# Performance work log

Hardware: AMD Instinct MI355X
Metric: run time of the kernel (lower is better)

Reference implementation:

```python
import jax, jax.numpy as jnp
import numpy as np

B, T, C, L = 1024, 1024, 96, 32
BLANK = C - 1          # tf.compat.v1.nn.ctc_loss uses num_classes-1 as blank
S = 2 * L + 1          # extended label length (blanks interleaved)
NEG = -1e30            # log-space 'zero'


def setup_inputs() -> dict:
    key = jax.random.key(0)
    k1, k2 = jax.random.split(key)
    y_true = jax.random.randint(k1, (B, L), 0, BLANK).astype(jnp.int64)  # labels in [0, C-2]
    y_pred = jax.random.normal(k2, (B, T, C), dtype=jnp.float32)          # pre-softmax logits
    return {"y_true": y_true, "y_pred": y_pred}


def _ctc_loss(y_pred, y_true):
    # y_pred: [B,T,C] logits, y_true: [B,L] int labels. All lengths are full
    # (label_length = L, input_length = T), matching the layer's call().
    logp = jax.nn.log_softmax(y_pred, axis=-1)                   # [B,T,C]
    # extended labels: blank, l0, blank, l1, ..., blank  -> [B,S]
    ext = jnp.full((B, S), BLANK, dtype=jnp.int32).at[:, 1::2].set(y_true.astype(jnp.int32))
    # skip transition allowed where ext[s] != blank and ext[s] != ext[s-2]
    skip = jnp.concatenate(
        [jnp.zeros((B, 2), bool), (ext[:, 2:] != BLANK) & (ext[:, 2:] != ext[:, :-2])],
        axis=1)                                                  # [B,S]
    # per-time emission log-probs of extended labels: [T,B,S]
    lp_ext = jnp.take_along_axis(logp, ext[:, None, :], axis=2)  # [B,T,S]
    lp_ext = jnp.transpose(lp_ext, (1, 0, 2))                    # [T,B,S]

    alpha0 = (jnp.full((B, S), NEG, dtype=logp.dtype)
              .at[:, 0].set(lp_ext[0, :, 0])
              .at[:, 1].set(lp_ext[0, :, 1]))

    def step(alpha, lp_t):
        a_stay = alpha
        a_prev = jnp.concatenate([jnp.full((B, 1), NEG, alpha.dtype), alpha[:, :-1]], axis=1)
        a_skip = jnp.concatenate([jnp.full((B, 2), NEG, alpha.dtype), alpha[:, :-2]], axis=1)
        a_skip = jnp.where(skip, a_skip, NEG)
        m = jnp.maximum(jnp.maximum(a_stay, a_prev), a_skip)
        new = m + jnp.log(jnp.exp(a_stay - m) + jnp.exp(a_prev - m) + jnp.exp(a_skip - m))
        return new + lp_t, None

    alphaT, _ = jax.lax.scan(step, alpha0, lp_ext[1:])
    # total log-likelihood ends at last blank or last label
    end = jnp.stack([alphaT[:, S - 1], alphaT[:, S - 2]], axis=0)  # [2,B]
    loss = -jax.scipy.special.logsumexp(end, axis=0)               # [B]
    return loss[:, None]                                           # [B,1], as ctc_batch_cost


def reference(y_true, y_pred):
    return _ctc_loss(y_pred, y_true)
```

## Files before the change

kernel.cpp:

```cpp
#include <hip/hip_runtime.h>


#define NB 1024
#define NT 1024
#define NC 96
#define NL 32
#define NEGF (-1e30f)
#define CHUNK 32
#define NCHUNK (NT / CHUNK)
#define SLOTF 97
#define LOG2E 1.4426950408889634f
#define LN2   0.69314718055994531f

__device__ __forceinline__ float fexp2(float x) { return __builtin_amdgcn_exp2f(x); }
__device__ __forceinline__ float flog2(float x) { return __builtin_amdgcn_logf(x); }

template <int CTRL>
__device__ __forceinline__ float dpp_mov(float v) {
  return __int_as_float(__builtin_amdgcn_update_dpp(
      __float_as_int(v), __float_as_int(v), CTRL, 0xF, 0xF, false));
}
__device__ __forceinline__ float dpp_shr1(float oldv, float v) {
  return __int_as_float(__builtin_amdgcn_update_dpp(
      __float_as_int(oldv), __float_as_int(v), 0x138, 0xF, 0xF, false));
}

__global__ __launch_bounds__(256) void ctc_fused(const int* __restrict__ yt,
                                                 const float* __restrict__ yp,
                                                 float* __restrict__ out) {
  __shared__ float ring[2 * CHUNK * SLOTF];

  const int b = blockIdx.x;
  const int wid = threadIdx.x >> 6;
  const int lane = threadIdx.x & 63;

  const float* __restrict__ xrow = yp + (size_t)b * NT * NC;

  const int cw = b & 3;
  const bool is_cons = (wid == cw);
  const int pr = ((wid - cw + 4) & 3) - 1;

  int extc = 95;
  bool skipf = false;
  if (is_cons) {
    const int* lab = yt + b * NL;
    if ((lane & 1) == 0) {
      const int j = lane >> 1;
      extc = lab[j];
      skipf = (j > 0) && (extc != lab[j - 1]);
    }
    __builtin_amdgcn_s_setprio(1);
  }

  const int rsel = lane >> 5;
  const int l32 = lane & 31;

  float UA[6][3], UB[6][3];

  auto load_regs = [&](float (&U)[6][3], int t0) {
    const float* rp = xrow + (size_t)(t0 + 2 * pr + rsel) * NC + l32;
#pragma unroll
    for (int jj = 0; jj < 6; ++jj) {
      if (pr + 3 * jj < 16) {
        U[jj][0] = rp[jj * 6 * NC + 0];
        U[jj][1] = rp[jj * 6 * NC + 32];
        U[jj][2] = rp[jj * 6 * NC + 64];
      }
    }
  };

  auto compute_store = [&](float (&U)[6][3], int cc) {
    float* wb = ring + (cc & 1) * (CHUNK * SLOTF) + (2 * pr + rsel) * SLOTF + l32;
#pragma unroll
    for (int jj = 0; jj < 6; ++jj) {
      if (pr + 3 * jj < 16) {
        const float u0 = U[jj][0] * LOG2E;
        const float u1 = U[jj][1] * LOG2E;
        const float u2 = U[jj][2] * LOG2E;
        float z = fexp2(u0) + fexp2(u1) + fexp2(u2);
        z += dpp_mov<0xB1>(z);
        z += dpp_mov<0x4E>(z);
        z += dpp_mov<0x124>(z);
        z += dpp_mov<0x128>(z);
        z += __shfl_xor(z, 16);
        const float lz = flog2(z);
        wb[jj * 6 * SLOTF + 0]  = u0 - lz;
        wb[jj * 6 * SLOTF + 32] = u1 - lz;
        wb[jj * 6 * SLOTF + 64] = u2 - lz;
      }
    }
  };

  float alpha = NEGF;
  float a0 = NEGF;

  auto consume = [&](int cc, bool first) {
    const float* hb = ring + (cc & 1) * (CHUNK * SLOTF) + extc;
    const float* hb95 = ring + (cc & 1) * (CHUNK * SLOTF) + 95;
    float lq[4], lqb[4];
    lq[0] = hb[0 * SLOTF];  lqb[0] = hb95[0 * SLOTF];
    lq[1] = hb[1 * SLOTF];  lqb[1] = hb95[1 * SLOTF];
    lq[2] = hb[2 * SLOTF];  lqb[2] = hb95[2 * SLOTF];
    lq[3] = 0.0f;           lqb[3] = 0.0f;
#pragma unroll
    for (int tt = 0; tt < CHUNK; ++tt) {
      const float lp = lq[tt & 3];
      const float lpb = lqb[tt & 3];
      if (tt + 3 < CHUNK) {
        lq[(tt + 3) & 3] = hb[(tt + 3) * SLOTF];
        lqb[(tt + 3) & 3] = hb95[(tt + 3) * SLOTF];
      }
      if (first && tt == 0) {
        a0 = lpb;
        alpha = (lane == 0) ? lp : NEGF;
      } else {
        const float ap = dpp_shr1(a0, alpha);
        float as = dpp_shr1(NEGF, ap);
        as = skipf ? as : NEGF;
        float mm, mid, mn;
        asm("v_max3_f32 %0, %1, %2, %3" : "=v"(mm) : "v"(alpha), "v"(ap), "v"(as));
        asm("v_med3_f32 %0, %1, %2, %3" : "=v"(mid) : "v"(alpha), "v"(ap), "v"(as));
        asm("v_min3_f32 %0, %1, %2, %3" : "=v"(mn) : "v"(alpha), "v"(ap), "v"(as));
        const float sm = (1.0f + fexp2(mid - mm)) + fexp2(mn - mm);
        alpha = (mm + lp) + flog2(sm);
        a0 += lpb;
      }
    }
  };

  if (!is_cons) load_regs(UA, 0);

  for (int c = 0; c < NCHUNK; c += 2) {
    if (!is_cons) {
      if (c + 1 < NCHUNK) load_regs(UB, (c + 1) * CHUNK);
      compute_store(UA, c);
      __syncthreads();
      if (c + 2 < NCHUNK) load_regs(UA, (c + 2) * CHUNK);
      compute_store(UB, c + 1);
      __syncthreads();
    } else {
      __syncthreads();
      if (c == 0) consume(0, true);
      else consume(c, false);
      __syncthreads();
      consume(c + 1, false);
    }
  }

  if (is_cons) {
    const float aS1 = __shfl(alpha, 63);
    const float aS2 = __shfl(alpha, 62);
    if (lane == 0) {
      const float mF = fmaxf(aS1, aS2);
      const float r = mF + flog2(fexp2(aS1 - mF) + fexp2(aS2 - mF));
      out[b] = -r * LN2;
    }
  }
}

extern "C" void kernel_launch(void* const* d_in, const int* in_sizes, int n_in,
                              void* d_out, int out_size, void* d_ws, size_t ws_size,
                              hipStream_t stream) {
  const int* yt = (const int*)d_in[0];
  const float* yp = (const float*)d_in[1];
  float* out = (float*)d_out;
  hipLaunchKernelGGL(ctc_fused, dim3(NB), dim3(256), 0, stream, yt, yp, out);
}
```

Measured before the change: 86.50 us.

## Gather extended-label log-probs in producers and store them as packed float2 rows

Measured after the change: 99.30 us. 14.8% more time.

```diff
diff --git a/kernel.cpp b/kernel.cpp
--- a/kernel.cpp
+++ b/kernel.cpp
@@ -8,7 +8,6 @@
 #define NEGF (-1e30f)
 #define CHUNK 32
 #define NCHUNK (NT / CHUNK)
-#define SLOTF 97
 #define LOG2E 1.4426950408889634f
 #define LN2   0.69314718055994531f
 
@@ -24,11 +23,17 @@
   return __int_as_float(__builtin_amdgcn_update_dpp(
       __float_as_int(oldv), __float_as_int(v), 0x138, 0xF, 0xF, false));
 }
+__device__ __forceinline__ float bperm(int byte_addr, float v) {
+  return __int_as_float(__builtin_amdgcn_ds_bpermute(byte_addr, __float_as_int(v)));
+}
+__device__ __forceinline__ float rdlane(float v, int l) {
+  return __int_as_float(__builtin_amdgcn_readlane(__float_as_int(v), l));
+}
 
 __global__ __launch_bounds__(256) void ctc_fused(const int* __restrict__ yt,
                                                  const float* __restrict__ yp,
                                                  float* __restrict__ out) {
-  __shared__ float ring[2 * CHUNK * SLOTF];
+  __shared__ float2 ring2[2 * CHUNK * 64];
 
   const int b = blockIdx.x;
   const int wid = threadIdx.x >> 6;
@@ -40,14 +45,19 @@
   const bool is_cons = (wid == cw);
   const int pr = ((wid - cw + 4) & 3) - 1;
 
-  int extc = 95;
+  const int* lab = yt + b * NL;
+  const int myl = lab[lane >> 1];
+  const int ea = ((lane & 1) == 0) ? myl : 95;
+  const bool e_hi = (ea >= 64);
+  const bool e_mid = (ea >= 32) && (ea < 64);
+  const int addrA = (ea & 31) << 2;
+  const int addrB = addrA + 128;
+
   bool skipf = false;
   if (is_cons) {
-    const int* lab = yt + b * NL;
     if ((lane & 1) == 0) {
       const int j = lane >> 1;
-      extc = lab[j];
-      skipf = (j > 0) && (extc != lab[j - 1]);
+      skipf = (j > 0) && (myl != lab[j - 1]);
     }
     __builtin_amdgcn_s_setprio(1);
   }
@@ -70,7 +80,7 @@
   };
 
   auto compute_store = [&](float (&U)[6][3], int cc) {
-    float* wb = ring + (cc & 1) * (CHUNK * SLOTF) + (2 * pr + rsel) * SLOTF + l32;
+    float2* wb = ring2 + (cc & 1) * (CHUNK * 64) + (2 * pr) * 64 + lane;
 #pragma unroll
     for (int jj = 0; jj < 6; ++jj) {
       if (pr + 3 * jj < 16) {
@@ -84,9 +94,27 @@
         z += dpp_mov<0x128>(z);
         z += __shfl_xor(z, 16);
         const float lz = flog2(z);
-        wb[jj * 6 * SLOTF + 0]  = u0 - lz;
-        wb[jj * 6 * SLOTF + 32] = u1 - lz;
-        wb[jj * 6 * SLOTF + 64] = u2 - lz;
+        const float v0 = u0 - lz, v1 = u1 - lz, v2 = u2 - lz;
+        {
+          const float r0 = bperm(addrA, v0), r1 = bperm(addrA, v1),
+                      r2 = bperm(addrA, v2);
+          float s = e_mid ? r1 : r0;
+          s = e_hi ? r2 : s;
+          float2 pr2;
+          pr2.x = s;
+          pr2.y = rdlane(v2, 31);
+          wb[jj * 6 * 64] = pr2;
+        }
+        {
+          const float r0 = bperm(addrB, v0), r1 = bperm(addrB, v1),
+                      r2 = bperm(addrB, v2);
+          float s = e_mid ? r1 : r0;
+          s = e_hi ? r2 : s;
+          float2 pr2;
+          pr2.x = s;
+          pr2.y = rdlane(v2, 63);
+          wb[jj * 6 * 64 + 64] = pr2;
+        }
       }
     }
   };
@@ -94,37 +122,40 @@
   float alpha = NEGF;
   float a0 = NEGF;
 
+  auto lse_step = [&](float lp, float lpb) {
+    const float ap = dpp_shr1(a0, alpha);
+    float as = dpp_shr1(NEGF, ap);
+    as = skipf ? as : NEGF;
+    float mm, mid, mn;
+    asm("v_max3_f32 %0, %1, %2, %3" : "=v"(mm) : "v"(alpha), "v"(ap), "v"(as));
+    asm("v_med3_f32 %0, %1, %2, %3" : "=v"(mid) : "v"(alpha), "v"(ap), "v"(as));
+    asm("v_min3_f32 %0, %1, %2, %3" : "=v"(mn) : "v"(alpha), "v"(ap), "v"(as));
+    const float sm = (1.0f + fexp2(mid - mm)) + fexp2(mn - mm);
+    alpha = (mm + lp) + flog2(sm);
+    a0 += lpb;
+  };
+
   auto consume = [&](int cc, bool first) {
-    const float* hb = ring + (cc & 1) * (CHUNK * SLOTF) + extc;
-    const float* hb95 = ring + (cc & 1) * (CHUNK * SLOTF) + 95;
-    float lq[4], lqb[4];
-    lq[0] = hb[0 * SLOTF];  lqb[0] = hb95[0 * SLOTF];
-    lq[1] = hb[1 * SLOTF];  lqb[1] = hb95[1 * SLOTF];
-    lq[2] = hb[2 * SLOTF];  lqb[2] = hb95[2 * SLOTF];
-    lq[3] = 0.0f;           lqb[3] = 0.0f;
+    const float2* hb = ring2 + (cc & 1) * (CHUNK * 64) + lane;
+    float2 q0 = hb[0 * 64];
+    float2 q1 = hb[1 * 64];
+    float2 q2 = hb[2 * 64];
+    float2 q3;
 #pragma unroll
-    for (int tt = 0; tt < CHUNK; ++tt) {
-      const float lp = lq[tt & 3];
-      const float lpb = lqb[tt & 3];
-      if (tt + 3 < CHUNK) {
-        lq[(tt + 3) & 3] = hb[(tt + 3) * SLOTF];
-        lqb[(tt + 3) & 3] = hb95[(tt + 3) * SLOTF];
+    for (int tt = 0; tt < CHUNK; tt += 4) {
+      if (tt + 3 < CHUNK) q3 = hb[(tt + 3) * 64];
+      if (first && tt == 0) {
+        a0 = q0.y;
+        alpha = (lane == 0) ? q0.x : NEGF;
+      } else {
+        lse_step(q0.x, q0.y);
       }
-      if (first && tt == 0) {
-        a0 = lpb;
-        alpha = (lane == 0) ? lp : NEGF;
-      } else {
-        const float ap = dpp_shr1(a0, alpha);
-        float as = dpp_shr1(NEGF, ap);
-        as = skipf ? as : NEGF;
-        float mm, mid, mn;
-        asm("v_max3_f32 %0, %1, %2, %3" : "=v"(mm) : "v"(alpha), "v"(ap), "v"(as));
-        asm("v_med3_f32 %0, %1, %2, %3" : "=v"(mid) : "v"(alpha), "v"(ap), "v"(as));
-        asm("v_min3_f32 %0, %1, %2, %3" : "=v"(mn) : "v"(alpha), "v"(ap), "v"(as));
-        const float sm = (1.0f + fexp2(mid - mm)) + fexp2(mn - mm);
-        alpha = (mm + lp) + flog2(sm);
-        a0 += lpb;
-      }
+      if (tt + 4 < CHUNK) q0 = hb[(tt + 4) * 64];
+      lse_step(q1.x, q1.y);
+      if (tt + 5 < CHUNK) q1 = hb[(tt + 5) * 64];
+      lse_step(q2.x, q2.y);
+      if (tt + 6 < CHUNK) q2 = hb[(tt + 6) * 64];
+      lse_step(q3.x, q3.y);
     }
   };
 
```

## Replace producer/consumer block with single-wave kernel using cross-lane gather

Applied to the files above, without the earlier changes.

Result: slower. 131.8 us (+52.3%).

```diff
diff --git a/kernel.cpp b/kernel.cpp
--- a/kernel.cpp
+++ b/kernel.cpp
@@ -8,7 +8,6 @@
 #define NEGF (-1e30f)
 #define CHUNK 32
 #define NCHUNK (NT / CHUNK)
-#define SLOTF 97
 #define LOG2E 1.4426950408889634f
 #define LN2   0.69314718055994531f
 
@@ -24,137 +23,135 @@
   return __int_as_float(__builtin_amdgcn_update_dpp(
       __float_as_int(oldv), __float_as_int(v), 0x138, 0xF, 0xF, false));
 }
+__device__ __forceinline__ float bperm(int byte_addr, float v) {
+  return __int_as_float(__builtin_amdgcn_ds_bpermute(byte_addr, __float_as_int(v)));
+}
+__device__ __forceinline__ float rdlane(float v, int l) {
+  return __int_as_float(__builtin_amdgcn_readlane(__float_as_int(v), l));
+}
 
-__global__ __launch_bounds__(256) void ctc_fused(const int* __restrict__ yt,
-                                                 const float* __restrict__ yp,
-                                                 float* __restrict__ out) {
-  __shared__ float ring[2 * CHUNK * SLOTF];
-
+__global__ __launch_bounds__(64, 1) void ctc_wave(const int* __restrict__ yt,
+                                                  const float* __restrict__ yp,
+                                                  float* __restrict__ out) {
   const int b = blockIdx.x;
-  const int wid = threadIdx.x >> 6;
-  const int lane = threadIdx.x & 63;
+  const int lane = threadIdx.x;
 
   const float* __restrict__ xrow = yp + (size_t)b * NT * NC;
+  const int* lab = yt + b * NL;
 
-  const int cw = b & 3;
-  const bool is_cons = (wid == cw);
-  const int pr = ((wid - cw + 4) & 3) - 1;
-
-  int extc = 95;
+  const int myl = lab[lane >> 1];
+  const int ea = ((lane & 1) == 0) ? myl : 95;
+  const int srcl = ea / 3;
+  const int comp = ea - 3 * srcl;
+  const bool m1 = (comp == 1);
+  const bool m2 = (comp == 2);
+  const int addrA = srcl << 2;
+  const int addrB = addrA + 128;
   bool skipf = false;
-  if (is_cons) {
-    const int* lab = yt + b * NL;
-    if ((lane & 1) == 0) {
-      const int j = lane >> 1;
-      extc = lab[j];
-      skipf = (j > 0) && (extc != lab[j - 1]);
-    }
-    __builtin_amdgcn_s_setprio(1);
+  if ((lane & 1) == 0) {
+    const int j = lane >> 1;
+    skipf = (j > 0) && (myl != lab[j - 1]);
   }
 
   const int rsel = lane >> 5;
   const int l32 = lane & 31;
 
-  float UA[6][3], UB[6][3];
+  float U_A[16][3], U_B[16][3];
 
-  auto load_regs = [&](float (&U)[6][3], int t0) {
-    const float* rp = xrow + (size_t)(t0 + 2 * pr + rsel) * NC + l32;
+  auto load_regs = [&](float (&U)[16][3], int t0) {
+    const float* rp = xrow + (size_t)(t0 + rsel) * NC + 3 * l32;
 #pragma unroll
-    for (int jj = 0; jj < 6; ++jj) {
-      if (pr + 3 * jj < 16) {
-        U[jj][0] = rp[jj * 6 * NC + 0];
-        U[jj][1] = rp[jj * 6 * NC + 32];
-        U[jj][2] = rp[jj * 6 * NC + 64];
-      }
+    for (int p = 0; p < 16; ++p) {
+      const float* q = rp + (size_t)(2 * p) * NC;
+      U[p][0] = q[0];
+      U[p][1] = q[1];
+      U[p][2] = q[2];
     }
   };
 
-  auto compute_store = [&](float (&U)[6][3], int cc) {
-    float* wb = ring + (cc & 1) * (CHUNK * SLOTF) + (2 * pr + rsel) * SLOTF + l32;
-#pragma unroll
-    for (int jj = 0; jj < 6; ++jj) {
-      if (pr + 3 * jj < 16) {
-        const float u0 = U[jj][0] * LOG2E;
-        const float u1 = U[jj][1] * LOG2E;
-        const float u2 = U[jj][2] * LOG2E;
-        float z = fexp2(u0) + fexp2(u1) + fexp2(u2);
-        z += dpp_mov<0xB1>(z);
-        z += dpp_mov<0x4E>(z);
-        z += dpp_mov<0x124>(z);
-        z += dpp_mov<0x128>(z);
-        z += __shfl_xor(z, 16);
-        const float lz = flog2(z);
-        wb[jj * 6 * SLOTF + 0]  = u0 - lz;
-        wb[jj * 6 * SLOTF + 32] = u1 - lz;
-        wb[jj * 6 * SLOTF + 64] = u2 - lz;
-      }
+  auto softgather = [&](const float (&u)[3], float& gA, float& bA_,
+                        float& gB, float& bB_) {
+    const float u0 = u[0] * LOG2E;
+    const float u1 = u[1] * LOG2E;
+    const float u2 = u[2] * LOG2E;
+    float z = fexp2(u0) + fexp2(u1) + fexp2(u2);
+    z += dpp_mov<0xB1>(z);
+    z += dpp_mov<0x4E>(z);
+    z += dpp_mov<0x124>(z);
+    z += dpp_mov<0x128>(z);
+    z += __shfl_xor(z, 16);
+    const float lz = flog2(z);
+    const float v0 = u0 - lz, v1 = u1 - lz, v2 = u2 - lz;
+    {
+      const float g0 = bperm(addrA, v0);
+      const float g1 = bperm(addrA, v1);
+      const float g2 = bperm(addrA, v2);
+      float s = m1 ? g1 : g0;
+      s = m2 ? g2 : s;
+      gA = s;
+      bA_ = rdlane(v2, 31);
+    }
+    {
+      const float g0 = bperm(addrB, v0);
+      const float g1 = bperm(addrB, v1);
+      const float g2 = bperm(addrB, v2);
+      float s = m1 ? g1 : g0;
+      s = m2 ? g2 : s;
+      gB = s;
+      bB_ = rdlane(v2, 63);
     }
   };
 
   float alpha = NEGF;
   float a0 = NEGF;
 
-  auto consume = [&](int cc, bool first) {
-    const float* hb = ring + (cc & 1) * (CHUNK * SLOTF) + extc;
-    const float* hb95 = ring + (cc & 1) * (CHUNK * SLOTF) + 95;
-    float lq[4], lqb[4];
-    lq[0] = hb[0 * SLOTF];  lqb[0] = hb95[0 * SLOTF];
-    lq[1] = hb[1 * SLOTF];  lqb[1] = hb95[1 * SLOTF];
-    lq[2] = hb[2 * SLOTF];  lqb[2] = hb95[2 * SLOTF];
-    lq[3] = 0.0f;           lqb[3] = 0.0f;
-#pragma unroll
-    for (int tt = 0; tt < CHUNK; ++tt) {
-      const float lp = lq[tt & 3];
-      const float lpb = lqb[tt & 3];
-      if (tt + 3 < CHUNK) {
-        lq[(tt + 3) & 3] = hb[(tt + 3) * SLOTF];
-        lqb[(tt + 3) & 3] = hb95[(tt + 3) * SLOTF];
-      }
-      if (first && tt == 0) {
-        a0 = lpb;
-        alpha = (lane == 0) ? lp : NEGF;
-      } else {
-        const float ap = dpp_shr1(a0, alpha);
-        float as = dpp_shr1(NEGF, ap);
-        as = skipf ? as : NEGF;
-        float mm, mid, mn;
-        asm("v_max3_f32 %0, %1, %2, %3" : "=v"(mm) : "v"(alpha), "v"(ap), "v"(as));
-        asm("v_med3_f32 %0, %1, %2, %3" : "=v"(mid) : "v"(alpha), "v"(ap), "v"(as));
-        asm("v_min3_f32 %0, %1, %2, %3" : "=v"(mn) : "v"(alpha), "v"(ap), "v"(as));
-        const float sm = (1.0f + fexp2(mid - mm)) + fexp2(mn - mm);
-        alpha = (mm + lp) + flog2(sm);
-        a0 += lpb;
-      }
-    }
+  auto lse_step = [&](float lp, float lpb) {
+    const float ap = dpp_shr1(a0, alpha);
+    float as = dpp_shr1(NEGF, ap);
+    as = skipf ? as : NEGF;
+    float mm, mid, mn;
+    asm("v_max3_f32 %0, %1, %2, %3" : "=v"(mm) : "v"(alpha), "v"(ap), "v"(as));
+    asm("v_med3_f32 %0, %1, %2, %3" : "=v"(mid) : "v"(alpha), "v"(ap), "v"(as));
+    asm("v_min3_f32 %0, %1, %2, %3" : "=v"(mn) : "v"(alpha), "v"(ap), "v"(as));
+    const float sm = (1.0f + fexp2(mid - mm)) + fexp2(mn - mm);
+    alpha = (mm + lp) + flog2(sm);
+    a0 += lpb;
   };
 
-  if (!is_cons) load_regs(UA, 0);
+  auto process = [&](const float (&U)[16][3], bool first) {
+    float gA, bA_, gB, bB_;
+    softgather(U[0], gA, bA_, gB, bB_);
+#pragma unroll
+    for (int p = 1; p < 16; ++p) {
+      float nA, nbA, nB, nbB;
+      softgather(U[p], nA, nbA, nB, nbB);
+      if (first && p == 1) {
+        a0 = bA_;
+        alpha = (lane == 0) ? gA : NEGF;
+      } else {
+        lse_step(gA, bA_);
+      }
+      lse_step(gB, bB_);
+      gA = nA; bA_ = nbA; gB = nB; bB_ = nbB;
+    }
+    lse_step(gA, bA_);
+    lse_step(gB, bB_);
+  };
 
+  load_regs(U_A, 0);
   for (int c = 0; c < NCHUNK; c += 2) {
-    if (!is_cons) {
-      if (c + 1 < NCHUNK) load_regs(UB, (c + 1) * CHUNK);
-      compute_store(UA, c);
-      __syncthreads();
-      if (c + 2 < NCHUNK) load_regs(UA, (c + 2) * CHUNK);
-      compute_store(UB, c + 1);
-      __syncthreads();
-    } else {
-      __syncthreads();
-      if (c == 0) consume(0, true);
-      else consume(c, false);
-      __syncthreads();
-      consume(c + 1, false);
-    }
+    load_regs(U_B, (c + 1) * CHUNK);
+    process(U_A, c == 0);
+    if (c + 2 < NCHUNK) load_regs(U_A, (c + 2) * CHUNK);
+    process(U_B, false);
   }
 
-  if (is_cons) {
-    const float aS1 = __shfl(alpha, 63);
-    const float aS2 = __shfl(alpha, 62);
-    if (lane == 0) {
-      const float mF = fmaxf(aS1, aS2);
-      const float r = mF + flog2(fexp2(aS1 - mF) + fexp2(aS2 - mF));
-      out[b] = -r * LN2;
-    }
+  const float aS1 = __shfl(alpha, 63);
+  const float aS2 = __shfl(alpha, 62);
+  if (lane == 0) {
+    const float mF = fmaxf(aS1, aS2);
+    const float r = mF + flog2(fexp2(aS1 - mF) + fexp2(aS2 - mF));
+    out[b] = -r * LN2;
   }
 }
 
@@ -164,5 +161,5 @@
   const int* yt = (const int*)d_in[0];
   const float* yp = (const float*)d_in[1];
   float* out = (float*)d_out;
-  hipLaunchKernelGGL(ctc_fused, dim3(NB), dim3(256), 0, stream, yt, yp, out);
+  hipLaunchKernelGGL(ctc_wave, dim3(NB), dim3(64), 0, stream, yt, yp, out);
 }
```

## Precompute two-step CTC transition coefficients in producer waves to halve serial recurrence

Applied to the files above, without the earlier changes.

Result: slower. 157.4 us (+82.0%).

```diff
diff --git a/kernel.cpp b/kernel.cpp
--- a/kernel.cpp
+++ b/kernel.cpp
@@ -7,8 +7,8 @@
 #define NL 32
 #define NEGF (-1e30f)
 #define CHUNK 32
+#define NP 16
 #define NCHUNK (NT / CHUNK)
-#define SLOTF 97
 #define LOG2E 1.4426950408889634f
 #define LN2   0.69314718055994531f
 
@@ -24,56 +24,71 @@
   return __int_as_float(__builtin_amdgcn_update_dpp(
       __float_as_int(oldv), __float_as_int(v), 0x138, 0xF, 0xF, false));
 }
+__device__ __forceinline__ int dpp_shr1_i(int oldv, int v) {
+  return __builtin_amdgcn_update_dpp(oldv, v, 0x138, 0xF, 0xF, false);
+}
+__device__ __forceinline__ float rdlane(float v, int l) {
+  return __int_as_float(__builtin_amdgcn_readlane(__float_as_int(v), l));
+}
 
 __global__ __launch_bounds__(256) void ctc_fused(const int* __restrict__ yt,
                                                  const float* __restrict__ yp,
                                                  float* __restrict__ out) {
-  __shared__ float ring[2 * CHUNK * SLOTF];
+  __shared__ float2 c01[2][NP][64];
+  __shared__ float2 c23[2][NP][64];
+  __shared__ float  c4a[2][NP][64];
+  __shared__ float  a0i[2][NP];
 
   const int b = blockIdx.x;
   const int wid = threadIdx.x >> 6;
   const int lane = threadIdx.x & 63;
 
   const float* __restrict__ xrow = yp + (size_t)b * NT * NC;
+  const int* lab = yt + b * NL;
 
   const int cw = b & 3;
   const bool is_cons = (wid == cw);
   const int pr = ((wid - cw + 4) & 3) - 1;
 
-  int extc = 95;
-  bool skipf = false;
-  if (is_cons) {
-    const int* lab = yt + b * NL;
-    if ((lane & 1) == 0) {
-      const int j = lane >> 1;
-      extc = lab[j];
-      skipf = (j > 0) && (extc != lab[j - 1]);
-    }
-    __builtin_amdgcn_s_setprio(1);
-  }
+  const int myl = lab[lane >> 1];
+  const int ea = ((lane & 1) == 0) ? myl : 95;
+  const bool sk_s = ((lane & 1) == 0) && ((lane >> 1) > 0) &&
+                    (myl != lab[(lane >> 1) - 1]);
+  const int sk0 = sk_s ? 1 : 0;
+  const int skm1 = dpp_shr1_i(0, sk0);
+  const int skm2 = dpp_shr1_i(0, skm1);
+  const bool b_skm1 = (skm1 != 0);
+  const bool b_sk24 = sk_s && (skm2 != 0);
+
+  if (is_cons) __builtin_amdgcn_s_setprio(1);
 
   const int rsel = lane >> 5;
   const int l32 = lane & 31;
 
   float UA[6][3], UB[6][3];
-
-  auto load_regs = [&](float (&U)[6][3], int t0) {
+  float GA[6][2], GB[6][2];
+
+  auto load_regs = [&](float (&U)[6][3], float (&G)[6][2], int t0) {
     const float* rp = xrow + (size_t)(t0 + 2 * pr + rsel) * NC + l32;
+    const float* gp = xrow + (size_t)(t0 + 2 * pr) * NC + ea;
 #pragma unroll
     for (int jj = 0; jj < 6; ++jj) {
-      if (pr + 3 * jj < 16) {
+      if (pr + 3 * jj < NP) {
         U[jj][0] = rp[jj * 6 * NC + 0];
         U[jj][1] = rp[jj * 6 * NC + 32];
         U[jj][2] = rp[jj * 6 * NC + 64];
-      }
-    }
-  };
-
-  auto compute_store = [&](float (&U)[6][3], int cc) {
-    float* wb = ring + (cc & 1) * (CHUNK * SLOTF) + (2 * pr + rsel) * SLOTF + l32;
+        G[jj][0] = gp[jj * 6 * NC];
+        G[jj][1] = gp[jj * 6 * NC + NC];
+      }
+    }
+  };
+
+  auto compute_store = [&](float (&U)[6][3], float (&G)[6][2], int cc) {
+    const int slot = cc & 1;
 #pragma unroll
     for (int jj = 0; jj < 6; ++jj) {
-      if (pr + 3 * jj < 16) {
+      const int p = pr + 3 * jj;
+      if (p < NP) {
         const float u0 = U[jj][0] * LOG2E;
         const float u1 = U[jj][1] * LOG2E;
         const float u2 = U[jj][2] * LOG2E;
@@ -84,9 +99,41 @@
         z += dpp_mov<0x128>(z);
         z += __shfl_xor(z, 16);
         const float lz = flog2(z);
-        wb[jj * 6 * SLOTF + 0]  = u0 - lz;
-        wb[jj * 6 * SLOTF + 32] = u1 - lz;
-        wb[jj * 6 * SLOTF + 64] = u2 - lz;
+        const float lzA = rdlane(lz, 0);
+        const float lzB = rdlane(lz, 32);
+        const float bA = rdlane(u2, 31) - lzA;
+        const float bB = rdlane(u2, 63) - lzB;
+        const float lp1 = G[jj][0] * LOG2E - lzA;
+        const float lp2 = G[jj][1] * LOG2E - lzB;
+        if (cc == 0 && p == 0) {
+          c01[slot][0][lane] = make_float2(lp1, lp2);
+          c23[slot][0][lane] = make_float2(bA, bB);
+          c4a[slot][0][lane] = NEGF;
+          if (lane == 0) a0i[slot][0] = 0.0f;
+        } else {
+          const float L1 = dpp_shr1(bA, lp1);
+          const float L2 = dpp_shr1(bA, L1);
+          const float mA = sk_s ? lp1 : NEGF;
+          const float mC = sk_s ? L2 : NEGF;
+          const float mB = b_skm1 ? L1 : NEGF;
+          const float mD = b_sk24 ? L2 : NEGF;
+          const float c0 = lp1 + lp2;
+          const float x1 = fmaxf(lp1, L1), y1 = fminf(lp1, L1);
+          const float c1 = (x1 + lp2) + flog2(1.0f + fexp2(y1 - x1));
+          float m3, md, mn;
+          asm("v_max3_f32 %0, %1, %2, %3" : "=v"(m3) : "v"(mA), "v"(L1), "v"(mC));
+          asm("v_med3_f32 %0, %1, %2, %3" : "=v"(md) : "v"(mA), "v"(L1), "v"(mC));
+          asm("v_min3_f32 %0, %1, %2, %3" : "=v"(mn) : "v"(mA), "v"(L1), "v"(mC));
+          const float c2 =
+              (m3 + lp2) + flog2((1.0f + fexp2(md - m3)) + fexp2(mn - m3));
+          const float x3 = fmaxf(mB, mC), y3 = fminf(mB, mC);
+          const float c3 = (x3 + lp2) + flog2(1.0f + fexp2(y3 - x3));
+          const float c4 = mD + lp2;
+          c01[slot][p][lane] = make_float2(c0, c1);
+          c23[slot][p][lane] = make_float2(c2, c3);
+          c4a[slot][p][lane] = c4;
+          if (lane == 0) a0i[slot][p] = bA + bB;
+        }
       }
     }
   };
@@ -94,49 +141,75 @@
   float alpha = NEGF;
   float a0 = NEGF;
 
+  auto lse_single = [&](float lp, float lpb) {
+    const float ap = dpp_shr1(a0, alpha);
+    float as = dpp_shr1(NEGF, ap);
+    as = sk_s ? as : NEGF;
+    float mm, mid, mn;
+    asm("v_max3_f32 %0, %1, %2, %3" : "=v"(mm) : "v"(alpha), "v"(ap), "v"(as));
+    asm("v_med3_f32 %0, %1, %2, %3" : "=v"(mid) : "v"(alpha), "v"(ap), "v"(as));
+    asm("v_min3_f32 %0, %1, %2, %3" : "=v"(mn) : "v"(alpha), "v"(ap), "v"(as));
+    const float sm = (1.0f + fexp2(mid - mm)) + fexp2(mn - mm);
+    alpha = (mm + lp) + flog2(sm);
+    a0 += lpb;
+  };
+
+  auto pair_step = [&](float2 A, float2 Bb, float C4, float I) {
+    const float a1 = dpp_shr1(a0, alpha);
+    const float a2 = dpp_shr1(NEGF, a1);
+    const float a3 = dpp_shr1(NEGF, a2);
+    const float a4 = dpp_shr1(NEGF, a3);
+    const float t0 = alpha + A.x;
+    const float t1 = a1 + A.y;
+    const float t2 = a2 + Bb.x;
+    const float t3 = a3 + Bb.y;
+    const float t4 = a4 + C4;
+    float mh, mm;
+    asm("v_max3_f32 %0, %1, %2, %3" : "=v"(mh) : "v"(t0), "v"(t1), "v"(t2));
+    asm("v_max3_f32 %0, %1, %2, %3" : "=v"(mm) : "v"(mh), "v"(t3), "v"(t4));
+    const float s = ((fexp2(t0 - mm) + fexp2(t1 - mm)) +
+                     (fexp2(t2 - mm) + fexp2(t3 - mm))) + fexp2(t4 - mm);
+    alpha = mm + flog2(s);
+    a0 += I;
+  };
+
   auto consume = [&](int cc, bool first) {
-    const float* hb = ring + (cc & 1) * (CHUNK * SLOTF) + extc;
-    const float* hb95 = ring + (cc & 1) * (CHUNK * SLOTF) + 95;
-    float lq[4], lqb[4];
-    lq[0] = hb[0 * SLOTF];  lqb[0] = hb95[0 * SLOTF];
-    lq[1] = hb[1 * SLOTF];  lqb[1] = hb95[1 * SLOTF];
-    lq[2] = hb[2 * SLOTF];  lqb[2] = hb95[2 * SLOTF];
-    lq[3] = 0.0f;           lqb[3] = 0.0f;
+    const int slot = cc & 1;
+    float2 qa[2] = {c01[slot][0][lane], c01[slot][1][lane]};
+    float2 qb[2] = {c23[slot][0][lane], c23[slot][1][lane]};
+    float qc[2] = {c4a[slot][0][lane], c4a[slot][1][lane]};
+    float qi[2] = {a0i[slot][0], a0i[slot][1]};
 #pragma unroll
-    for (int tt = 0; tt < CHUNK; ++tt) {
-      const float lp = lq[tt & 3];
-      const float lpb = lqb[tt & 3];
-      if (tt + 3 < CHUNK) {
-        lq[(tt + 3) & 3] = hb[(tt + 3) * SLOTF];
-        lqb[(tt + 3) & 3] = hb95[(tt + 3) * SLOTF];
-      }
-      if (first && tt == 0) {
-        a0 = lpb;
-        alpha = (lane == 0) ? lp : NEGF;
+    for (int p = 0; p < NP; ++p) {
+      const float2 A = qa[p & 1];
+      const float2 Bb = qb[p & 1];
+      const float C4 = qc[p & 1];
+      const float I = qi[p & 1];
+      if (p + 2 < NP) {
+        qa[p & 1] = c01[slot][p + 2][lane];
+        qb[p & 1] = c23[slot][p + 2][lane];
+        qc[p & 1] = c4a[slot][p + 2][lane];
+        qi[p & 1] = a0i[slot][p + 2];
+      }
+      if (first && p == 0) {
+        a0 = Bb.x;
+        alpha = (lane == 0) ? A.x : NEGF;
+        lse_single(A.y, Bb.y);
       } else {
-        const float ap = dpp_shr1(a0, alpha);
-        float as = dpp_shr1(NEGF, ap);
-        as = skipf ? as : NEGF;
-        float mm, mid, mn;
-        asm("v_max3_f32 %0, %1, %2, %3" : "=v"(mm) : "v"(alpha), "v"(ap), "v"(as));
-        asm("v_med3_f32 %0, %1, %2, %3" : "=v"(mid) : "v"(alpha), "v"(ap), "v"(as));
-        asm("v_min3_f32 %0, %1, %2, %3" : "=v"(mn) : "v"(alpha), "v"(ap), "v"(as));
-        const float sm = (1.0f + fexp2(mid - mm)) + fexp2(mn - mm);
-        alpha = (mm + lp) + flog2(sm);
-        a0 += lpb;
-      }
-    }
-  };
-
-  if (!is_cons) load_regs(UA, 0);
+        pair_step(A, Bb, C4, I);
+      }
+    }
+  };
+
+  if (!is_cons) load_regs(UA, GA, 0);
 
   for (int c = 0; c < NCHUNK; c += 2) {
     if (!is_cons) {
-      if (c + 1 < NCHUNK) load_regs(UB, (c + 1) * CHUNK);
-      compute_store(UA, c);
-      __syncthreads();
-      if (c + 2 < NCHUNK) load_regs(UA, (c + 2) * CHUNK);
-      compute_store(UB, c + 1);
+      if (c + 1 < NCHUNK) load_regs(UB, GB, (c + 1) * CHUNK);
+      compute_store(UA, GA, c);
+      __syncthreads();
+      if (c + 2 < NCHUNK) load_regs(UA, GA, (c + 2) * CHUNK);
+      compute_store(UB, GB, c + 1);
       __syncthreads();
     } else {
       __syncthreads();
```
